# Kernel optimization log

Measured on AMD Instinct MI355X. Metric: run time of the kernel, lower is better.

## Reference

```python
import jax, jax.numpy as jnp
import numpy as np

N_QUBITS = 22
DIM = 2 ** N_QUBITS


def setup_inputs() -> dict:
    key = jax.random.key(0)
    k1, k2, k3, k4 = jax.random.split(key, 4)
    state = jax.random.normal(k1, (DIM,), dtype=jnp.float32)
    state = state / jnp.linalg.norm(state)
    rabi = jax.random.uniform(k2, (N_QUBITS,), dtype=jnp.float32)
    detune = jax.random.uniform(k3, (N_QUBITS,), dtype=jnp.float32)
    # U = triu(normal^2, k=1) flattened upper triangle -> interaction strengths
    U_params = jax.random.normal(k4, (N_QUBITS * (N_QUBITS - 1) // 2,), dtype=jnp.float32) ** 2
    return {"state": state, "rabi": rabi, "detune": detune, "U_params": U_params}


def reference(state, rabi, detune, U_params):
    # H|psi> = sum_i (rabi_i/2) X_i |psi> + sum_i (-detune_i) N_i |psi>
    #        + sum_{i<j} U_ij N_i N_j |psi>
    n = rabi.shape[0]
    dim = state.shape[0]
    # bit value of qubit i for each basis index k (qubit 0 = most significant,
    # matching state.reshape((2,)*n) axis ordering)
    idx = jnp.arange(dim, dtype=jnp.uint32)
    shifts = jnp.arange(n - 1, -1, -1, dtype=jnp.uint32)
    bits = ((idx[:, None] >> shifts[None, :]) & 1).astype(state.dtype)  # [dim, n]
    iu, ju = np.triu_indices(n, k=1)
    Umat = jnp.zeros((n, n), dtype=state.dtype).at[iu, ju].set(U_params)
    # diagonal part: detuning (Number ops) + pairwise interactions (N_i N_j)
    diag = bits @ (-detune) + jnp.sum((bits @ Umat) * bits, axis=1)  # [dim]
    out = diag * state
    # off-diagonal Rabi part: X_i flips qubit i
    st = state.reshape((2,) * n)
    for i in range(n):
        out = out + (0.5 * rabi[i]) * jnp.flip(st, axis=i).reshape(-1)
    return out
```

## Files before the change

kernel.cpp:

```cpp
#include <hip/hip_runtime.h>


#define THREADS 512
#define NBLK 512

__device__ __forceinline__ int uidx(int i, int j) {
    return i * (43 - i) / 2 + (j - i - 1);
}

__global__ __launch_bounds__(THREADS, 2) void ryd_kernel(
        const float* __restrict__ state, const float* __restrict__ rabi,
        const float* __restrict__ detune, const float* __restrict__ U,
        float* __restrict__ out) {
    __shared__ float4 tileS[2048];
    __shared__ float  dloS[2048];
    __shared__ float  Us[231];
    __shared__ float  dets[22];
    __shared__ float  CJ[4][11];
    __shared__ float  S4[4];

    const float4* __restrict__ sF4 = (const float4*)state;
    float4* __restrict__ oF4 = (float4*)out;
    const unsigned t = threadIdx.x;
    const unsigned blk = blockIdx.x;
    const unsigned tile = ((blk & 7u) << 6) | (blk >> 3);

    if (t < 231u) Us[t] = U[t];
    else if (t < 253u) dets[t - 231u] = detune[t - 231u];
    __syncthreads();

#pragma unroll
    for (int r = 0; r < 4; ++r) {
        const unsigned m = t + 512u * (unsigned)r;
        float s = 0.f;
        for (int j2 = 0; j2 < 11; ++j2) {
            if ((m >> j2) & 1u) {
                s -= dets[21 - j2];
                for (int j1 = 0; j1 < j2; ++j1)
                    if ((m >> j1) & 1u) s += Us[uidx(21 - j2, 21 - j1)];
            }
        }
        dloS[m] = s;
    }
    if (t < 44u) {
        const int c = (int)t / 11, j = (int)t % 11;
        const unsigned h = (tile << 2) | (unsigned)c;
        float cc = 0.f;
        for (int jh = 0; jh < 11; ++jh)
            if ((h >> jh) & 1u) cc += Us[uidx(10 - jh, 21 - j)];
        CJ[c][j] = cc;
    } else if (t < 48u) {
        const int c = (int)t - 44;
        const unsigned h = (tile << 2) | (unsigned)c;
        float s = 0.f;
        for (int j2 = 0; j2 < 11; ++j2) {
            if ((h >> j2) & 1u) {
                s -= dets[10 - j2];
                for (int j1 = 0; j1 < j2; ++j1)
                    if ((h >> j1) & 1u) s += Us[uidx(10 - j2, 10 - j1)];
            }
        }
        S4[c] = s;
    }

    float4 vreg[4];
#pragma unroll
    for (int c = 0; c < 4; ++c) {
        const unsigned f = t + 512u * (unsigned)c;
        vreg[c] = sF4[tile * 2048u + f];
        tileS[f] = vreg[c];
    }
    __syncthreads();

    const float r0 = 0.5f * rabi[21];
    const float r1 = 0.5f * rabi[20];
    float cb[9];
#pragma unroll
    for (int b = 0; b < 9; ++b) cb[b] = 0.5f * rabi[8 - b];

#pragma unroll
    for (int c = 0; c < 4; ++c) {
        const unsigned f = t + 512u * (unsigned)c;
        const unsigned F = tile * 2048u + f;
        float4 pg[9];
#pragma unroll
        for (int b = 0; b < 9; ++b)
            pg[b] = sF4[F ^ (2048u << b)];

        float cj[11];
#pragma unroll
        for (int j = 0; j < 11; ++j) cj[j] = CJ[c][j];
        float s = S4[c];
        const unsigned m = f & 511u;
#pragma unroll
        for (int j = 0; j < 9; ++j)
            s += ((m >> j) & 1u) ? cj[j + 2] : 0.f;
        const float4 dl = ((const float4*)dloS)[m];
        const float4 v = vreg[c];
        const float d0 = s + dl.x;
        const float d1 = s + cj[0] + dl.y;
        const float d2 = s + cj[1] + dl.z;
        const float d3 = s + cj[0] + cj[1] + dl.w;
        float4 acc;
        acc.x = d0 * v.x; acc.y = d1 * v.y; acc.z = d2 * v.z; acc.w = d3 * v.w;
        acc.x += r0 * v.y; acc.y += r0 * v.x; acc.z += r0 * v.w; acc.w += r0 * v.z;
        acc.x += r1 * v.z; acc.y += r1 * v.w; acc.z += r1 * v.x; acc.w += r1 * v.y;
#pragma unroll
        for (int b = 2; b <= 12; ++b) {
            const float rb = 0.5f * rabi[21 - b];
            const float4 p = tileS[f ^ (1u << (b - 2))];
            acc.x += rb * p.x; acc.y += rb * p.y; acc.z += rb * p.z; acc.w += rb * p.w;
        }
#pragma unroll
        for (int b = 0; b < 9; ++b) {
            acc.x += cb[b] * pg[b].x; acc.y += cb[b] * pg[b].y;
            acc.z += cb[b] * pg[b].z; acc.w += cb[b] * pg[b].w;
        }
        oF4[F] = acc;
    }
}

extern "C" void kernel_launch(void* const* d_in, const int* in_sizes, int n_in,
                              void* d_out, int out_size, void* d_ws, size_t ws_size,
                              hipStream_t stream) {
    const float* state  = (const float*)d_in[0];
    const float* rabi   = (const float*)d_in[1];
    const float* detune = (const float*)d_in[2];
    const float* U      = (const float*)d_in[3];
    float* out = (float*)d_out;
    (void)in_sizes; (void)n_in; (void)out_size; (void)d_ws; (void)ws_size;

    hipLaunchKernelGGL(ryd_kernel, dim3(NBLK), dim3(THREADS), 0, stream,
                       state, rabi, detune, U, out);
}
```

Before: 25.58 us.

## Prefetch far-partner loads across chunks, factor diagonal table, use nontemporal stores

Moves the tile loads and the first chunk's three farthest-partner global loads ahead of the first barrier. Each later chunk now prefetches those three loads for the next chunk into a double buffer, to hide global latency. The per-thread diagonal table now computes its four entries from one shared 9-bit base plus closed-form corrections for the two top bits, instead of four full loops. Output writes use nontemporal stores, and launch bounds now ask for 4 blocks per CU. The prefetch buffers and the higher occupancy target add register pressure and could cause spills.

```diff
diff --git a/kernel.cpp b/kernel.cpp
--- a/kernel.cpp
+++ b/kernel.cpp
@@ -4,43 +4,64 @@
 #define THREADS 512
 #define NBLK 512
 
+typedef float fvec4 __attribute__((ext_vector_type(4)));
+
 __device__ __forceinline__ int uidx(int i, int j) {
     return i * (43 - i) / 2 + (j - i - 1);
 }
 
-__global__ __launch_bounds__(THREADS, 2) void ryd_kernel(
+__global__ __launch_bounds__(THREADS, 4) void ryd_kernel(
         const float* __restrict__ state, const float* __restrict__ rabi,
         const float* __restrict__ detune, const float* __restrict__ U,
         float* __restrict__ out) {
     __shared__ float4 tileS[2048];
-    __shared__ float  dloS[2048];
-    __shared__ float  Us[231];
-    __shared__ float  dets[22];
-    __shared__ float  CJ[4][11];
-    __shared__ float  S4[4];
+    __shared__ __align__(16) float dloS[2048];
+    __shared__ float Us[231];
+    __shared__ float dets[22];
+    __shared__ float CJ[4][11];
+    __shared__ float S4v[4];
 
     const float4* __restrict__ sF4 = (const float4*)state;
     float4* __restrict__ oF4 = (float4*)out;
     const unsigned t = threadIdx.x;
     const unsigned blk = blockIdx.x;
     const unsigned tile = ((blk & 7u) << 6) | (blk >> 3);
+    const unsigned tbase = tile * 2048u;
 
     if (t < 231u) Us[t] = U[t];
     else if (t < 253u) dets[t - 231u] = detune[t - 231u];
+
+    float4 vreg[4];
+#pragma unroll
+    for (int c = 0; c < 4; ++c)
+        vreg[c] = sF4[tbase + t + 512u * (unsigned)c];
+    float4 pgl[2][3];
+#pragma unroll
+    for (int b = 6; b < 9; ++b)
+        pgl[0][b - 6] = sF4[(tbase + t) ^ (2048u << b)];
+
     __syncthreads();
 
+    {
+        float base = 0.f, R9 = 0.f, R10 = 0.f;
 #pragma unroll
-    for (int r = 0; r < 4; ++r) {
-        const unsigned m = t + 512u * (unsigned)r;
-        float s = 0.f;
-        for (int j2 = 0; j2 < 11; ++j2) {
-            if ((m >> j2) & 1u) {
-                s -= dets[21 - j2];
+        for (int j2 = 0; j2 < 9; ++j2) {
+            if ((t >> j2) & 1u) {
+                base -= dets[21 - j2];
+#pragma unroll
                 for (int j1 = 0; j1 < j2; ++j1)
-                    if ((m >> j1) & 1u) s += Us[uidx(21 - j2, 21 - j1)];
+                    if ((t >> j1) & 1u) base += Us[uidx(21 - j2, 21 - j1)];
+                R9  += Us[uidx(12, 21 - j2)];
+                R10 += Us[uidx(11, 21 - j2)];
             }
         }
-        dloS[m] = s;
+        const float w9  = -dets[12];
+        const float w10 = -dets[11];
+        const float u910 = Us[uidx(11, 12)];
+        dloS[t]         = base;
+        dloS[t + 512u]  = base + w9 + R9;
+        dloS[t + 1024u] = base + w10 + R10;
+        dloS[t + 1536u] = base + w9 + R9 + w10 + R10 + u910;
     }
     if (t < 44u) {
         const int c = (int)t / 11, j = (int)t % 11;
@@ -60,16 +81,12 @@
                     if ((h >> j1) & 1u) s += Us[uidx(10 - j2, 10 - j1)];
             }
         }
-        S4[c] = s;
+        S4v[c] = s;
     }
 
-    float4 vreg[4];
 #pragma unroll
-    for (int c = 0; c < 4; ++c) {
-        const unsigned f = t + 512u * (unsigned)c;
-        vreg[c] = sF4[tile * 2048u + f];
-        tileS[f] = vreg[c];
-    }
+    for (int c = 0; c < 4; ++c)
+        tileS[t + 512u * (unsigned)c] = vreg[c];
     __syncthreads();
 
     const float r0 = 0.5f * rabi[21];
@@ -81,16 +98,21 @@
 #pragma unroll
     for (int c = 0; c < 4; ++c) {
         const unsigned f = t + 512u * (unsigned)c;
-        const unsigned F = tile * 2048u + f;
-        float4 pg[9];
+        const unsigned F = tbase + f;
+        if (c < 3) {
 #pragma unroll
-        for (int b = 0; b < 9; ++b)
+            for (int b = 6; b < 9; ++b)
+                pgl[(c + 1) & 1][b - 6] = sF4[(F + 512u) ^ (2048u << b)];
+        }
+        float4 pg[6];
+#pragma unroll
+        for (int b = 0; b < 6; ++b)
             pg[b] = sF4[F ^ (2048u << b)];
 
         float cj[11];
 #pragma unroll
         for (int j = 0; j < 11; ++j) cj[j] = CJ[c][j];
-        float s = S4[c];
+        float s = S4v[c];
         const unsigned m = f & 511u;
 #pragma unroll
         for (int j = 0; j < 9; ++j)
@@ -112,11 +134,19 @@
             acc.x += rb * p.x; acc.y += rb * p.y; acc.z += rb * p.z; acc.w += rb * p.w;
         }
 #pragma unroll
-        for (int b = 0; b < 9; ++b) {
+        for (int b = 0; b < 6; ++b) {
             acc.x += cb[b] * pg[b].x; acc.y += cb[b] * pg[b].y;
             acc.z += cb[b] * pg[b].z; acc.w += cb[b] * pg[b].w;
         }
-        oF4[F] = acc;
+#pragma unroll
+        for (int q = 0; q < 3; ++q) {
+            const float4 p = pgl[c & 1][q];
+            acc.x += cb[6 + q] * p.x; acc.y += cb[6 + q] * p.y;
+            acc.z += cb[6 + q] * p.z; acc.w += cb[6 + q] * p.w;
+        }
+        union { float4 s4; fvec4 v4; } u;
+        u.s4 = acc;
+        __builtin_nontemporal_store(u.v4, reinterpret_cast<fvec4*>(oF4 + F));
     }
 }
 
```

Result: faster. 20.92 us (-18.2%).
